# Performance work log

Hardware: AMD Instinct MI355X
Metric: run time of the kernel (lower is better)

Reference implementation:

```python
import jax, jax.numpy as jnp
import numpy as np

N = 100000          # nodes
E = 1600000         # edges
ND = 38             # n_discrete_features
NC = 90             # total continuous features (3 time slices)
NCS = NC // 3       # continuous features per slice
CH = 4              # n_channels_c
NH = 128            # n_hidden
NH0 = ND - 6 + 3 * CH   # 44
NH1 = NH0 + NH          # 172
L_CROSS = 2


def _leaky(x):
    return jax.nn.leaky_relu(x, 0.01)


def setup_inputs() -> dict:
    key = jax.random.key(0)
    ks = jax.random.split(key, 16)
    def w(k, shape, fan_in):
        return jax.random.normal(k, shape, jnp.float32) * (1.0 / np.sqrt(fan_in).astype(np.float32))
    return {
        "discrete_x": jax.random.randint(ks[0], (N, ND), 0, 2),
        "continous_x": jax.random.normal(ks[1], (N, NC), jnp.float32),
        "edge_index": jax.random.randint(ks[2], (2, E), 0, N),
        "edge_attr": jax.random.normal(ks[3], (E, 1), jnp.float32),
        "churn_date": jax.random.randint(ks[4], (N,), 0, 365),
        "emb_c_W": w(ks[5], (NCS, CH), NCS), "emb_c_b": jnp.zeros((CH,), jnp.float32),
        "g0_W": w(ks[6], (NH0, NH), NH0), "g0_b": jnp.zeros((NH,), jnp.float32),
        "gcn1_W": w(ks[7], (NH, NH), NH), "gcn1_b": jnp.zeros((NH,), jnp.float32),
        "gcn2_W": w(ks[8], (NH, NH), NH), "gcn2_b": jnp.zeros((NH,), jnp.float32),
        "dnn_W1": w(ks[9], (NH1, NH1), NH1), "dnn_b1": jnp.zeros((NH1,), jnp.float32),
        "dnn_W2": w(ks[10], (NH1, NH1), NH1), "dnn_b2": jnp.zeros((NH1,), jnp.float32),
        "cross_w": w(ks[11], (L_CROSS, NH1), NH1), "cross_b": jnp.zeros((L_CROSS, NH1), jnp.float32),
        "pred_W1": w(ks[12], (2 * NH1, NH1), 2 * NH1), "pred_b1": jnp.zeros((NH1,), jnp.float32),
        "pred_W2": w(ks[13], (NH1, 1), NH1), "pred_b2": jnp.zeros((1,), jnp.float32),
    }


def reference(discrete_x, continous_x, edge_index, edge_attr, churn_date,
              emb_c_W, emb_c_b, g0_W, g0_b, gcn1_W, gcn1_b, gcn2_W, gcn2_b,
              dnn_W1, dnn_b1, dnn_W2, dnn_b2, cross_w, cross_b,
              pred_W1, pred_b1, pred_W2, pred_b2):
    # --- discrete embedding: collapse leading 7-way one-hot block to one index column -> [N, ND-6]
    dow = jnp.argmax(discrete_x[:, :7], axis=-1).astype(jnp.float32)[:, None]
    x_d = jnp.concatenate([dow, discrete_x[:, 7:].astype(jnp.float32)], axis=-1)
    # --- continuous embedding: 3 time slices, per-slice linear to CH channels -> [N, 3*CH]
    x_c = (continous_x.reshape(-1, 3, NCS) @ emb_c_W + emb_c_b).reshape(-1, 3 * CH)
    # --- graph branch
    x_g = _leaky(jnp.concatenate([x_d, x_c], axis=-1) @ g0_W + g0_b)  # [N, NH]
    src, dst = edge_index[0], edge_index[1]
    deg = jax.ops.segment_sum(jnp.ones((E,), jnp.float32), dst, num_segments=N) + 1.0  # self-loops
    dis = jax.lax.rsqrt(deg)
    def gcn(x, W, b):
        xw = x @ W
        msg = xw[src] * (dis[src] * dis[dst])[:, None]          # [E, NH]
        agg = jax.ops.segment_sum(msg, dst, num_segments=N)
        agg = agg + xw / deg[:, None]                           # self-loop term
        return agg + b
    x_g = _leaky(gcn(x_g, gcn1_W, gcn1_b))
    x_g = _leaky(gcn(x_g, gcn2_W, gcn2_b))
    # --- fusion
    x = jnp.concatenate([x_d, x_c, x_g], axis=-1)  # [N, NH1]
    x_deep = _leaky(_leaky(x @ dnn_W1 + dnn_b1) @ dnn_W2 + dnn_b2)
    x0 = x
    xl = x
    for i in range(L_CROSS):
        xl = x0 * (xl @ cross_w[i])[:, None] + cross_b[i] + xl
    h = jnp.concatenate([x_deep, xl], axis=-1)  # [N, 2*NH1]
    return jax.nn.sigmoid(_leaky(h @ pred_W1 + pred_b1) @ pred_W2 + pred_b2)  # [N, 1]
```

## Files before the change

kernel.cpp:

```cpp
#include <hip/hip_runtime.h>
#include <math.h>


typedef __attribute__((ext_vector_type(8))) _Float16 f16x8;
typedef __attribute__((ext_vector_type(4))) _Float16 f16x4;
typedef __attribute__((ext_vector_type(2))) _Float16 f16x2;
typedef __attribute__((ext_vector_type(4))) float f32x4;

__device__ __forceinline__ float leakyf(float v) { return v > 0.f ? v : 0.01f * v; }

#define MFMA16(a, b, c) __builtin_amdgcn_mfma_f32_16x16x32_f16((a), (b), (c), 0, 0, 0)
#define AGG_SCALE 1048576.0f
#define AGG_INV   9.5367431640625e-07f

__global__ __launch_bounds__(256) void cnt_edge_kernel(const int* __restrict__ dst,
                                                       int* __restrict__ cnt, int E)
{
    int i = blockIdx.x * 256 + threadIdx.x;
    if (i < E) atomicAdd(&cnt[dst[i]], 1);
}

__global__ __launch_bounds__(256) void scan1_kernel(const int* __restrict__ cnt,
                                                    int* __restrict__ incl,
                                                    int* __restrict__ bsum, int N)
{
    __shared__ int s[256];
    int tid = threadIdx.x;
    int i = blockIdx.x * 256 + tid;
    s[tid] = (i < N) ? cnt[i] : 0;
    __syncthreads();
    #pragma unroll
    for (int off = 1; off < 256; off <<= 1) {
        int t = (tid >= off) ? s[tid - off] : 0;
        __syncthreads();
        s[tid] += t;
        __syncthreads();
    }
    if (i < N) incl[i] = s[tid];
    if (tid == 255) bsum[blockIdx.x] = s[255];
}

__global__ void scan2_kernel(int* __restrict__ bsum, int nb)
{
    int lane = threadIdx.x & 63;
    int run = 0;
    for (int base = 0; base < nb; base += 64) {
        int i = base + lane;
        int orig = (i < nb) ? bsum[i] : 0;
        int v = orig;
        #pragma unroll
        for (int off = 1; off < 64; off <<= 1) {
            int t = __shfl_up(v, off, 64);
            if (lane >= off) v += t;
        }
        if (i < nb) bsum[i] = run + v - orig;
        run += __shfl(v, 63, 64);
    }
}

__global__ __launch_bounds__(256) void scan3_kernel(const int* __restrict__ incl,
                                                    const int* __restrict__ cnt,
                                                    const int* __restrict__ bsum,
                                                    int* __restrict__ row_ptr,
                                                    int* __restrict__ cursor,
                                                    float* __restrict__ dis, int N)
{
    int i = blockIdx.x * 256 + threadIdx.x;
    if (i < N) {
        int v = incl[i] - cnt[i] + bsum[i >> 8];
        row_ptr[i] = v;
        cursor[i] = v;
        dis[i] = rsqrtf((float)cnt[i] + 1.0f);
    }
}

__global__ __launch_bounds__(256) void fill_kernel(const int* __restrict__ src,
                                                   const int* __restrict__ dst,
                                                   const float* __restrict__ dis,
                                                   int* __restrict__ cursor,
                                                   int2* __restrict__ colcf, int E)
{
    int e = blockIdx.x * 256 + threadIdx.x;
    if (e < E) {
        int s = src[e], d = dst[e];
        int p = atomicAdd(&cursor[d], 1);
        colcf[p] = make_int2(s, __float_as_int(dis[s] * dis[d]));
    }
}

__global__ __launch_bounds__(256) void wprep_kernel(
    const float* __restrict__ gcn1_W, const float* __restrict__ gcn2_W,
    const float* __restrict__ dnn_W1, const float* __restrict__ dnn_W2,
    const float* __restrict__ pred_W1,
    const float* __restrict__ cb, const float* __restrict__ cw,
    _Float16* __restrict__ G1f, _Float16* __restrict__ G2f,
    _Float16* __restrict__ W1f, _Float16* __restrict__ W2f,
    _Float16* __restrict__ Paf, _Float16* __restrict__ Pbf,
    float* __restrict__ cvec)
{
    int b = blockIdx.x;
    if (b == 704) {
        int col = threadIdx.x;
        if (col < 176) {
            float s = 0.f;
            if (col < 172)
                for (int k = 0; k < 172; ++k)
                    s += (cb[k] + cb[172 + k]) * pred_W1[(size_t)(172 + k) * 172 + col];
            cvec[col] = s;
        } else if (col == 176) {
            float c = 0.f;
            for (int k = 0; k < 172; ++k) c += cb[k] * cw[172 + k];
            cvec[176] = c;
        }
        return;
    }
    const float* W; _Float16* Wf; int K, Ncol, NT, base;
    if (b < 64)       { W = gcn1_W; Wf = G1f; K = 128; Ncol = 128; NT = 8;  base = 0;   }
    else if (b < 128) { W = gcn2_W; Wf = G2f; K = 128; Ncol = 128; NT = 8;  base = 64;  }
    else if (b < 272) { W = dnn_W1; Wf = W1f; K = 172; Ncol = 172; NT = 12; base = 128; }
    else if (b < 416) { W = dnn_W2; Wf = W2f; K = 172; Ncol = 172; NT = 12; base = 272; }
    else if (b < 560) { W = pred_W1; Wf = Paf; K = 172; Ncol = 172; NT = 12; base = 416; }
    else              { W = pred_W1 + (size_t)172 * 172; Wf = Pbf; K = 172; Ncol = 172; NT = 12; base = 560; }
    int idx = (b - base) * 256 + threadIdx.x;
    int e = idx & 7;
    int lane = (idx >> 3) & 63;
    int ct = idx >> 9;
    int t = ct % NT, c = ct / NT;
    int col = t * 16 + (lane & 15);
    int k = c * 32 + (lane >> 4) * 8 + e;
    float x = (k < K && col < Ncol) ? W[(size_t)k * Ncol + col] : 0.f;
    Wf[idx] = (_Float16)x;
}

__global__ __launch_bounds__(256) void g0_kernel(
    const int* __restrict__ disc, const float* __restrict__ cont,
    const float* __restrict__ Wc, const float* __restrict__ bc,
    const float* __restrict__ W, const float* __restrict__ bias,
    float* __restrict__ xg, _Float16* __restrict__ sh, int N)
{
    constexpr int TM = 32, K = 44, RB = 8;
    __shared__ float Alds[TM][K];
    __shared__ float Wlds[K][128];
    const int tid = threadIdx.x, lane = tid & 63, wv = tid >> 6;
    const int row0 = blockIdx.x * TM;

    for (int idx = tid; idx < TM * 38; idx += 256) {
        int r = idx / 38, j = idx - r * 38;
        int row = row0 + r;
        if (j == 0) {
            float o = 0.f;
            if (row < N) {
                const int* dr = disc + (size_t)row * 38;
                int best = dr[0], bi = 0;
                #pragma unroll
                for (int q = 1; q < 7; ++q) { int v = dr[q]; if (v > best) { best = v; bi = q; } }
                o = (float)bi;
            }
            Alds[r][0] = o;
        } else if (j >= 7) {
            Alds[r][j - 6] = (row < N) ? (float)disc[(size_t)row * 38 + j] : 0.f;
        }
    }
    for (int idx = tid; idx < TM * 12; idx += 256) {
        int r = idx / 12, q = idx - r * 12;
        int t = q >> 2, ch = q & 3;
        int row = row0 + r;
        float s = 0.f;
        if (row < N) {
            s = bc[ch];
            const float* cr = cont + (size_t)row * 90 + t * 30;
            #pragma unroll
            for (int j = 0; j < 30; ++j) s += cr[j] * Wc[j * 4 + ch];
        }
        Alds[r][32 + t * 4 + ch] = s;
    }
    for (int idx = tid; idx < K * 32; idx += 256) {
        int k = idx >> 5, c4 = idx & 31;
        ((float4*)&Wlds[k][0])[c4] = ((const float4*)W)[idx];
    }
    __syncthreads();

    float acc[RB][2];
    float b0 = bias[lane], b1 = bias[lane + 64];
    #pragma unroll
    for (int r = 0; r < RB; ++r) { acc[r][0] = b0; acc[r][1] = b1; }

    for (int k = 0; k < K; ++k) {
        float w0 = Wlds[k][lane], w1 = Wlds[k][lane + 64];
        #pragma unroll
        for (int r = 0; r < RB; ++r) {
            float a = Alds[wv * RB + r][k];
            acc[r][0] += a * w0;
            acc[r][1] += a * w1;
        }
    }
    #pragma unroll
    for (int r = 0; r < RB; ++r) {
        int row = row0 + wv * RB + r;
        if (row < N) {
            float v0 = leakyf(acc[r][0]);
            float v1 = leakyf(acc[r][1]);
            xg[(size_t)row * 128 + lane]      = v0;
            xg[(size_t)row * 128 + lane + 64] = v1;
            sh[(size_t)row * 128 + lane]      = (_Float16)v0;
            sh[(size_t)row * 128 + lane + 64] = (_Float16)v1;
        }
    }
}

__global__ __launch_bounds__(512, 4) void gcn_fused(
    const _Float16* __restrict__ shin, float* __restrict__ xio,
    const int2* __restrict__ colcf,
    const int* __restrict__ rowp, const int* __restrict__ rend,
    const float* __restrict__ dis, const _Float16* __restrict__ B,
    const float* __restrict__ bias, _Float16* __restrict__ shout,
    int write_f32, int N)
{
    __shared__ __attribute__((aligned(16))) _Float16 Xs[64][136];
    const int tid = threadIdx.x, lane = tid & 63, wv = tid >> 6;
    const int l15 = lane & 15, kq = lane >> 4;
    const int row0 = blockIdx.x * 64;
    const f16x2* S2 = (const f16x2*)shin;
    const float2* X2 = (const float2*)xio;

    #pragma unroll 1
    for (int rr = 0; rr < 8; ++rr) {
        const int r = (wv << 3) + rr;
        const int row = row0 + r;
        float ox = 0.f, oy = 0.f;
        if (row < N) {
            int i = rowp[row], en = rend[row];
            long long iax = 0, iay = 0;
            for (; i + 7 < en; i += 8) {
                int2 ee[8];
                f16x2 vv[8];
                #pragma unroll
                for (int u = 0; u < 8; ++u) ee[u] = colcf[i + u];
                #pragma unroll
                for (int u = 0; u < 8; ++u) vv[u] = S2[(size_t)ee[u].x * 64 + lane];
                #pragma unroll
                for (int u = 0; u < 8; ++u) {
                    float cf = __int_as_float(ee[u].y) * AGG_SCALE;
                    iax += __float2int_rn((float)vv[u].x * cf);
                    iay += __float2int_rn((float)vv[u].y * cf);
                }
            }
            for (; i < en; ++i) {
                int2 e = colcf[i];
                f16x2 v = S2[(size_t)e.x * 64 + lane];
                float cf = __int_as_float(e.y) * AGG_SCALE;
                iax += __float2int_rn((float)v.x * cf);
                iay += __float2int_rn((float)v.y * cf);
            }
            float ax = (float)iax * AGG_INV;
            float ay = (float)iay * AGG_INV;
            float dn = dis[row];
            float2 sv = X2[(size_t)row * 64 + lane];
            float d2 = dn * dn;
            ox = ax + sv.x * d2;
            oy = ay + sv.y * d2;
        }
        f16x2 h = { (_Float16)ox, (_Float16)oy };
        *(f16x2*)&Xs[r][lane * 2] = h;
    }
    __syncthreads();

    const int msub = wv >> 1, half = wv & 1;
    f32x4 acc[4];
    #pragma unroll
    for (int t = 0; t < 4; ++t) acc[t] = (f32x4){0.f, 0.f, 0.f, 0.f};

    #pragma unroll
    for (int c = 0; c < 4; ++c) {
        f16x8 a = *(const f16x8*)&Xs[msub * 16 + l15][c * 32 + kq * 8];
        #pragma unroll
        for (int t = 0; t < 4; ++t) {
            int tg = half * 4 + t;
            f16x8 b = *(const f16x8*)(B + (((size_t)c * 8 + tg) * 64 + lane) * 8);
            acc[t] = MFMA16(a, b, acc[t]);
        }
    }

    #pragma unroll
    for (int t = 0; t < 4; ++t) {
        int col = (half * 4 + t) * 16 + l15;
        float bb = bias[col];
        #pragma unroll
        for (int r = 0; r < 4; ++r) {
            int row = row0 + msub * 16 + kq * 4 + r;
            if (row < N) {
                float v = leakyf(acc[t][r] + bb);
                if (write_f32) xio[(size_t)row * 128 + col] = v;
                shout[(size_t)row * 128 + col] = (_Float16)v;
            }
        }
    }
}

__device__ __forceinline__ void gemm_pass6(
    const _Float16 (*X)[200], const _Float16* __restrict__ B,
    f32x4* acc, int msub, int half, int l15, int kq, int lane)
{
    #pragma unroll
    for (int t = 0; t < 6; ++t) acc[t] = (f32x4){0.f, 0.f, 0.f, 0.f};
    #pragma unroll
    for (int c = 0; c < 6; ++c) {
        f16x8 a = *(const f16x8*)&X[msub * 16 + l15][c * 32 + kq * 8];
        #pragma unroll
        for (int t = 0; t < 6; ++t) {
            f16x8 b = *(const f16x8*)(B + (((size_t)c * 12 + half * 6 + t) * 64 + lane) * 8);
            acc[t] = MFMA16(a, b, acc[t]);
        }
    }
}

__global__ __launch_bounds__(512, 3) void tail_kernel(
    const int* __restrict__ disc, const float* __restrict__ cont,
    const float* __restrict__ Wc, const float* __restrict__ bc,
    const _Float16* __restrict__ sh,
    const _Float16* __restrict__ W1, const float* __restrict__ b1,
    const _Float16* __restrict__ W2, const float* __restrict__ b2,
    const _Float16* __restrict__ Pa, const _Float16* __restrict__ Pb,
    const float* __restrict__ pb1,
    const float* __restrict__ cw, const float* __restrict__ cvec,
    const float* __restrict__ pw2, const float* __restrict__ pb2,
    float* __restrict__ out, int N)
{
    __shared__ __attribute__((aligned(16))) _Float16 Xs[64][200];
    __shared__ __attribute__((aligned(16))) _Float16 Ts[64][200];
    __shared__ float als[64];
    __shared__ float partial[64][2];
    const int tid = threadIdx.x, lane = tid & 63, wv = tid >> 6;
    const int msub = wv >> 1, half = wv & 1, l15 = lane & 15, kq = lane >> 4;
    const int row0 = blockIdx.x * 64;

    float* TsF = (float*)&Ts[0][0];
    for (int idx = tid; idx < 64 * 45; idx += 512) {
        int r = idx / 45, j2 = idx - r * 45;
        int row = row0 + r;
        float2 v = make_float2(0.f, 0.f);
        if (row < N) v = ((const float2*)(cont + (size_t)row * 90))[j2];
        TsF[r * 100 + j2 * 2]     = v.x;
        TsF[r * 100 + j2 * 2 + 1] = v.y;
    }
    __syncthreads();

    for (int idx = tid; idx < 64 * 44; idx += 512) {
        int r = idx / 44, j = idx - r * 44;
        int row = row0 + r;
        float v = 0.f;
        if (row < N) {
            if (j == 0) {
                const int* dr = disc + (size_t)row * 38;
                int best = dr[0], bi = 0;
                #pragma unroll
                for (int q = 1; q < 7; ++q) { int t = dr[q]; if (t > best) { best = t; bi = q; } }
                v = (float)bi;
            } else if (j < 32) {
                v = (float)disc[(size_t)row * 38 + j + 6];
            } else {
                int q = j - 32, t = q >> 2, ch = q & 3;
                float s = bc[ch];
                const float* crl = &TsF[r * 100 + t * 30];
                #pragma unroll
                for (int kk = 0; kk < 30; ++kk) s += crl[kk] * Wc[kk * 4 + ch];
                v = s;
            }
        }
        Xs[r][j] = (_Float16)v;
    }
    for (int idx = tid; idx < 64 * 32; idx += 512) {
        int r = idx >> 5, q = idx & 31;
        int row = row0 + r;
        uint2 v = {0u, 0u};
        if (row < N) v = *(const uint2*)(sh + (size_t)row * 128 + q * 4);
        *(uint2*)&Xs[r][44 + q * 4] = v;
    }
    for (int idx = tid; idx < 64 * 28; idx += 512) {
        int r = idx / 28, j = idx - r * 28;
        Xs[r][172 + j] = (_Float16)0.f;
    }
    __syncthreads();

    {
        int row = tid >> 3, sub = tid & 7;
        float d1 = 0.f, d2 = 0.f;
        for (int col = sub; col < 172; col += 8) {
            float x = (float)Xs[row][col];
            d1 += x * cw[col];
            d2 += x * cw[172 + col];
        }
        #pragma unroll
        for (int off = 1; off < 8; off <<= 1) {
            d1 += __shfl_xor(d1, off, 64);
            d2 += __shfl_xor(d2, off, 64);
        }
        if (sub == 0) {
            float a1 = 1.f + d1;
            als[row] = a1 + a1 * d2 + cvec[176];
        }
    }

    f32x4 accA[6], accB[6];

    gemm_pass6(Xs, W1, accA, msub, half, l15, kq, lane);
    #pragma unroll
    for (int t = 0; t < 6; ++t) {
        int col = half * 96 + t * 16 + l15;
        #pragma unroll
        for (int r = 0; r < 4; ++r) {
            int row = msub * 16 + kq * 4 + r;
            float v = (col < 172) ? leakyf(accA[t][r] + b1[col]) : 0.f;
            Ts[row][col] = (_Float16)v;
        }
    }
    __syncthreads();
    gemm_pass6(Ts, W2, accA, msub, half, l15, kq, lane);
    __syncthreads();
    #pragma unroll
    for (int t = 0; t < 6; ++t) {
        int col = half * 96 + t * 16 + l15;
        #pragma unroll
        for (int r = 0; r < 4; ++r) {
            int row = msub * 16 + kq * 4 + r;
            float v = (col < 172) ? leakyf(accA[t][r] + b2[col]) : 0.f;
            Ts[row][col] = (_Float16)v;
        }
    }
    __syncthreads();

    gemm_pass6(Ts, Pa, accA, msub, half, l15, kq, lane);
    gemm_pass6(Xs, Pb, accB, msub, half, l15, kq, lane);

    float part[4] = {0.f, 0.f, 0.f, 0.f};
    #pragma unroll
    for (int t = 0; t < 6; ++t) {
        int col = half * 96 + t * 16 + l15;
        if (col < 172) {
            float cv = cvec[col] + pb1[col], w2v = pw2[col];
            #pragma unroll
            for (int r = 0; r < 4; ++r) {
                int row = msub * 16 + kq * 4 + r;
                float pre = accA[t][r] + als[row] * accB[t][r] + cv;
                part[r] += leakyf(pre) * w2v;
            }
        }
    }
    #pragma unroll
    for (int r = 0; r < 4; ++r) {
        #pragma unroll
        for (int off = 1; off < 16; off <<= 1)
            part[r] += __shfl_xor(part[r], off, 64);
    }
    if (l15 == 0) {
        #pragma unroll
        for (int r = 0; r < 4; ++r)
            partial[msub * 16 + kq * 4 + r][half] = part[r];
    }
    __syncthreads();
    if (tid < 64) {
        int grow = row0 + tid;
        if (grow < N) {
            float s = partial[tid][0] + partial[tid][1] + pb2[0];
            out[grow] = 1.f / (1.f + expf(-s));
        }
    }
}

extern "C" void kernel_launch(void* const* d_in, const int* in_sizes, int n_in,
                              void* d_out, int out_size, void* d_ws, size_t ws_size,
                              hipStream_t stream)
{
    const int*   disc    = (const int*)d_in[0];
    const float* cont    = (const float*)d_in[1];
    const int*   eidx    = (const int*)d_in[2];
    const float* emb_W   = (const float*)d_in[5];
    const float* emb_b   = (const float*)d_in[6];
    const float* g0_W    = (const float*)d_in[7];
    const float* g0_b    = (const float*)d_in[8];
    const float* gcn1_W  = (const float*)d_in[9];
    const float* gcn1_b  = (const float*)d_in[10];
    const float* gcn2_W  = (const float*)d_in[11];
    const float* gcn2_b  = (const float*)d_in[12];
    const float* dnn_W1  = (const float*)d_in[13];
    const float* dnn_b1  = (const float*)d_in[14];
    const float* dnn_W2  = (const float*)d_in[15];
    const float* dnn_b2  = (const float*)d_in[16];
    const float* cross_w = (const float*)d_in[17];
    const float* cross_b = (const float*)d_in[18];
    const float* pred_W1 = (const float*)d_in[19];
    const float* pred_b1 = (const float*)d_in[20];
    const float* pred_W2 = (const float*)d_in[21];
    const float* pred_b2 = (const float*)d_in[22];

    const int N = in_sizes[0] / 38;
    const int E = in_sizes[2] / 2;
    const int* src = eidx;
    const int* dst = eidx + E;

    float* xgF     = (float*)d_ws;
    _Float16* shA  = (_Float16*)(xgF + (size_t)128 * N);
    _Float16* shB  = shA + (size_t)128 * N;
    float* dis  = (float*)(shB + (size_t)128 * N);
    int* cnt    = (int*)(dis + N);
    int* rowp   = cnt + N;
    int* curs   = rowp + N;
    int* bsum   = curs + N;
    int2* colcf = (int2*)(((size_t)(bsum + 512) + 15) & ~(size_t)15);
    _Float16* wf = (_Float16*)(colcf + E);
    _Float16* G1f = wf;
    _Float16* G2f = G1f + 16384;
    _Float16* W1f = G2f + 16384;
    _Float16* W2f = W1f + 36864;
    _Float16* Paf = W2f + 36864;
    _Float16* Pbf = Paf + 36864;
    float* cvec   = (float*)(Pbf + 36864);

    auto cdiv = [](int a, int b) { return (a + b - 1) / b; };
    const int nb = cdiv(N, 256);

    wprep_kernel<<<705, 256, 0, stream>>>(
        gcn1_W, gcn2_W, dnn_W1, dnn_W2, pred_W1, cross_b, cross_w,
        G1f, G2f, W1f, W2f, Paf, Pbf, cvec);

    hipMemsetAsync(cnt, 0, (size_t)N * sizeof(int), stream);
    cnt_edge_kernel<<<cdiv(E, 256), 256, 0, stream>>>(dst, cnt, E);
    scan1_kernel<<<nb, 256, 0, stream>>>(cnt, curs, bsum, N);
    scan2_kernel<<<1, 64, 0, stream>>>(bsum, nb);
    scan3_kernel<<<nb, 256, 0, stream>>>(curs, cnt, bsum, rowp, curs, dis, N);
    fill_kernel<<<cdiv(E, 256), 256, 0, stream>>>(src, dst, dis, curs, colcf, E);

    g0_kernel<<<cdiv(N, 32), 256, 0, stream>>>(disc, cont, emb_W, emb_b, g0_W, g0_b,
                                               xgF, shA, N);

    gcn_fused<<<cdiv(N, 64), 512, 0, stream>>>(shA, xgF, colcf, rowp, curs, dis,
                                               G1f, gcn1_b, shB, 1, N);
    gcn_fused<<<cdiv(N, 64), 512, 0, stream>>>(shB, xgF, colcf, rowp, curs, dis,
                                               G2f, gcn2_b, shA, 0, N);

    tail_kernel<<<cdiv(N, 64), 512, 0, stream>>>(
        disc, cont, emb_W, emb_b, shA,
        W1f, dnn_b1, W2f, dnn_b2, Paf, Pbf, pred_b1,
        cross_w, cvec, pred_W2, pred_b2, (float*)d_out, N);
}
```

Baseline: 568.3 us.

## Fuse second GCN layer into the tail kernel

Moves the second GCN aggregation and its 128x128 MFMA transform into the start of the tail kernel. The result goes straight into the shared-memory feature tile, so one launch is removed along with the fp16 write and reread of the layer-2 output. In exchange the tail kernel gets longer and uses more registers, and it adds barriers that separate the reuse of the Ts and Xs tiles. The first GCN layer now always writes its fp32 output.

```diff
diff --git a/kernel.cpp b/kernel.cpp
--- a/kernel.cpp
+++ b/kernel.cpp
@@ -213,8 +213,7 @@
     const int2* __restrict__ colcf,
     const int* __restrict__ rowp, const int* __restrict__ rend,
     const float* __restrict__ dis, const _Float16* __restrict__ B,
-    const float* __restrict__ bias, _Float16* __restrict__ shout,
-    int write_f32, int N)
+    const float* __restrict__ bias, _Float16* __restrict__ shout, int N)
 {
     __shared__ __attribute__((aligned(16))) _Float16 Xs[64][136];
     const int tid = threadIdx.x, lane = tid & 63, wv = tid >> 6;
@@ -290,7 +289,7 @@
             int row = row0 + msub * 16 + kq * 4 + r;
             if (row < N) {
                 float v = leakyf(acc[t][r] + bb);
-                if (write_f32) xio[(size_t)row * 128 + col] = v;
+                xio[(size_t)row * 128 + col] = v;
                 shout[(size_t)row * 128 + col] = (_Float16)v;
             }
         }
@@ -317,7 +316,11 @@
 __global__ __launch_bounds__(512, 3) void tail_kernel(
     const int* __restrict__ disc, const float* __restrict__ cont,
     const float* __restrict__ Wc, const float* __restrict__ bc,
-    const _Float16* __restrict__ sh,
+    const _Float16* __restrict__ shB, const float* __restrict__ xgF,
+    const int2* __restrict__ colcf,
+    const int* __restrict__ rowp, const int* __restrict__ rend,
+    const float* __restrict__ dis,
+    const _Float16* __restrict__ G2, const float* __restrict__ g2b,
     const _Float16* __restrict__ W1, const float* __restrict__ b1,
     const _Float16* __restrict__ W2, const float* __restrict__ b2,
     const _Float16* __restrict__ Pa, const _Float16* __restrict__ Pb,
@@ -333,6 +336,79 @@
     const int tid = threadIdx.x, lane = tid & 63, wv = tid >> 6;
     const int msub = wv >> 1, half = wv & 1, l15 = lane & 15, kq = lane >> 4;
     const int row0 = blockIdx.x * 64;
+
+    {
+        const f16x2* S2 = (const f16x2*)shB;
+        const float2* X2 = (const float2*)xgF;
+        #pragma unroll 1
+        for (int rr = 0; rr < 8; ++rr) {
+            const int r = (wv << 3) + rr;
+            const int row = row0 + r;
+            float ox = 0.f, oy = 0.f;
+            if (row < N) {
+                int i = rowp[row], en = rend[row];
+                long long iax = 0, iay = 0;
+                for (; i + 7 < en; i += 8) {
+                    int2 ee[8];
+                    f16x2 vv[8];
+                    #pragma unroll
+                    for (int u = 0; u < 8; ++u) ee[u] = colcf[i + u];
+                    #pragma unroll
+                    for (int u = 0; u < 8; ++u) vv[u] = S2[(size_t)ee[u].x * 64 + lane];
+                    #pragma unroll
+                    for (int u = 0; u < 8; ++u) {
+                        float cf = __int_as_float(ee[u].y) * AGG_SCALE;
+                        iax += __float2int_rn((float)vv[u].x * cf);
+                        iay += __float2int_rn((float)vv[u].y * cf);
+                    }
+                }
+                for (; i < en; ++i) {
+                    int2 e = colcf[i];
+                    f16x2 v = S2[(size_t)e.x * 64 + lane];
+                    float cf = __int_as_float(e.y) * AGG_SCALE;
+                    iax += __float2int_rn((float)v.x * cf);
+                    iay += __float2int_rn((float)v.y * cf);
+                }
+                float ax = (float)iax * AGG_INV;
+                float ay = (float)iay * AGG_INV;
+                float dn = dis[row];
+                float2 sv = X2[(size_t)row * 64 + lane];
+                float d2 = dn * dn;
+                ox = ax + sv.x * d2;
+                oy = ay + sv.y * d2;
+            }
+            f16x2 h = { (_Float16)ox, (_Float16)oy };
+            *(f16x2*)&Ts[r][lane * 2] = h;
+        }
+    }
+    __syncthreads();
+
+    {
+        f32x4 acc[4];
+        #pragma unroll
+        for (int t = 0; t < 4; ++t) acc[t] = (f32x4){0.f, 0.f, 0.f, 0.f};
+        #pragma unroll
+        for (int c = 0; c < 4; ++c) {
+            f16x8 a = *(const f16x8*)&Ts[msub * 16 + l15][c * 32 + kq * 8];
+            #pragma unroll
+            for (int t = 0; t < 4; ++t) {
+                int tg = half * 4 + t;
+                f16x8 b = *(const f16x8*)(G2 + (((size_t)c * 8 + tg) * 64 + lane) * 8);
+                acc[t] = MFMA16(a, b, acc[t]);
+            }
+        }
+        #pragma unroll
+        for (int t = 0; t < 4; ++t) {
+            int col = (half * 4 + t) * 16 + l15;
+            float bb = g2b[col];
+            #pragma unroll
+            for (int r = 0; r < 4; ++r) {
+                int row = msub * 16 + kq * 4 + r;
+                Xs[row][44 + col] = (_Float16)leakyf(acc[t][r] + bb);
+            }
+        }
+    }
+    __syncthreads();
 
     float* TsF = (float*)&Ts[0][0];
     for (int idx = tid; idx < 64 * 45; idx += 512) {
@@ -369,13 +445,6 @@
         }
         Xs[r][j] = (_Float16)v;
     }
-    for (int idx = tid; idx < 64 * 32; idx += 512) {
-        int r = idx >> 5, q = idx & 31;
-        int row = row0 + r;
-        uint2 v = {0u, 0u};
-        if (row < N) v = *(const uint2*)(sh + (size_t)row * 128 + q * 4);
-        *(uint2*)&Xs[r][44 + q * 4] = v;
-    }
     for (int idx = tid; idx < 64 * 28; idx += 512) {
         int r = idx / 28, j = idx - r * 28;
         Xs[r][172 + j] = (_Float16)0.f;
@@ -400,10 +469,12 @@
             als[row] = a1 + a1 * d2 + cvec[176];
         }
     }
+    __syncthreads();
 
     f32x4 accA[6], accB[6];
 
     gemm_pass6(Xs, W1, accA, msub, half, l15, kq, lane);
+    __syncthreads();
     #pragma unroll
     for (int t = 0; t < 6; ++t) {
         int col = half * 96 + t * 16 + l15;
@@ -534,12 +605,10 @@
                                                xgF, shA, N);
 
     gcn_fused<<<cdiv(N, 64), 512, 0, stream>>>(shA, xgF, colcf, rowp, curs, dis,
-                                               G1f, gcn1_b, shB, 1, N);
-    gcn_fused<<<cdiv(N, 64), 512, 0, stream>>>(shB, xgF, colcf, rowp, curs, dis,
-                                               G2f, gcn2_b, shA, 0, N);
+                                               G1f, gcn1_b, shB, N);
 
     tail_kernel<<<cdiv(N, 64), 512, 0, stream>>>(
-        disc, cont, emb_W, emb_b, shA,
-        W1f, dnn_b1, W2f, dnn_b2, Paf, Pbf, pred_b1,
+        disc, cont, emb_W, emb_b, shB, xgF, colcf, rowp, curs, dis,
+        G2f, gcn2_b, W1f, dnn_b1, W2f, dnn_b2, Paf, Pbf, pred_b1,
         cross_w, cvec, pred_W2, pred_b2, (float*)d_out, N);
 }
```

Result: slower. 618.7 us (+8.9%).
